# Kernel optimization log

Measured on AMD Instinct MI355X. Metric: run time of the kernel, lower is better.

The kernel has to match this reference:

```python
import jax, jax.numpy as jnp
import numpy as np

N, E, R, G = 50000, 800000, 8, 128
IN_EMBD, LAYER, OUT = 64, 256, 256
CARDS = [33, 5, 3, 4, 2, 3]
EPS = 1e-5


def setup_inputs() -> dict:
    key = jax.random.key(0)
    ks = iter(jax.random.split(key, 40))
    d = {}
    # int inputs
    cols = [jax.random.randint(next(ks), (N,), 0, c) for c in CARDS]
    d['x'] = jnp.stack(cols, axis=1)                                  # [N,6]
    d['edge_index'] = jax.random.randint(next(ks), (2, E), 0, N)      # [2,E]
    d['edge_type'] = jax.random.randint(next(ks), (E,), 0, R)         # [E]
    d['batch'] = jnp.sort(jax.random.randint(next(ks), (N,), 0, G))   # [N]
    # embedding tables
    for i, c in enumerate(CARDS):
        d[f'emb{i}'] = jax.random.normal(next(ks), (c, IN_EMBD), jnp.float32)
    # RGCNConv1
    d['W1'] = jax.random.normal(next(ks), (R, 6 * IN_EMBD, LAYER), jnp.float32) * 0.05
    d['root1'] = jax.random.normal(next(ks), (6 * IN_EMBD, LAYER), jnp.float32) * 0.05
    d['b1'] = jnp.zeros((LAYER,), jnp.float32)
    # RGCNConv2
    d['W2'] = jax.random.normal(next(ks), (R, LAYER, OUT), jnp.float32) * 0.05
    d['root2'] = jax.random.normal(next(ks), (LAYER, OUT), jnp.float32) * 0.05
    d['b2'] = jnp.zeros((OUT,), jnp.float32)
    # gate_nn: Linear -> BatchNorm1d -> ReLU -> Linear(.,1)
    d['Wg1'] = jax.random.normal(next(ks), (OUT, OUT), jnp.float32) * 0.05
    d['bg1'] = jnp.zeros((OUT,), jnp.float32)
    d['gamma'] = jnp.ones((OUT,), jnp.float32)
    d['beta'] = jnp.zeros((OUT,), jnp.float32)
    d['Wg2'] = jax.random.normal(next(ks), (OUT, 1), jnp.float32) * 0.05
    d['bg2'] = jnp.zeros((1,), jnp.float32)
    # graph head
    d['Wgl'] = jax.random.normal(next(ks), (OUT, 1), jnp.float32) * 0.05
    d['bgl'] = jnp.zeros((1,), jnp.float32)
    return d


def rgcn_conv(h, src, dst, etype, W, root, b):
    # per-relation transform of all nodes, then gather per edge (avoids per-edge weight gather)
    hr = jnp.einsum('ni,rio->rno', h, W)            # [R,N,out]
    msg = hr[etype, src]                             # [E,out]
    # mean aggregation per (dst, relation), matching PyG RGCNConv default aggr='mean'
    counts = jnp.zeros((h.shape[0], W.shape[0]), h.dtype).at[dst, etype].add(1.0)
    norm = 1.0 / jnp.clip(counts, 1.0)               # [N,R]
    agg = jax.ops.segment_sum(msg * norm[dst, etype][:, None], dst, num_segments=h.shape[0])
    return agg + h @ root + b


def global_attention(x, batch, Wg1, bg1, gamma, beta, Wg2, bg2):
    h = x @ Wg1 + bg1
    mu = jnp.mean(h, axis=0)
    var = jnp.var(h, axis=0)
    h = (h - mu) * jax.lax.rsqrt(var + EPS) * gamma + beta   # BatchNorm1d (batch stats)
    gate = jax.nn.relu(h) @ Wg2 + bg2                        # [N,1]
    gmax = jax.ops.segment_max(gate, batch, num_segments=G)
    e = jnp.exp(gate - gmax[batch])
    denom = jax.ops.segment_sum(e, batch, num_segments=G)
    alpha = e / denom[batch]
    return jax.ops.segment_sum(alpha * x, batch, num_segments=G)  # [G,out]


def reference(x, edge_index, edge_type, batch,
              emb0, emb1, emb2, emb3, emb4, emb5,
              W1, root1, b1, W2, root2, b2,
              Wg1, bg1, gamma, beta, Wg2, bg2, Wgl, bgl):
    tables = [emb0, emb1, emb2, emb3, emb4, emb5]
    h = jnp.concatenate([tables[i][x[:, i]] for i in range(6)], axis=1)  # [N, 6*in_embd]
    src, dst = edge_index[0], edge_index[1]
    h = jax.nn.sigmoid(rgcn_conv(h, src, dst, edge_type, W1, root1, b1))
    h = jax.nn.sigmoid(rgcn_conv(h, src, dst, edge_type, W2, root2, b2))
    pooled = global_attention(h, batch, Wg1, bg1, gamma, beta, Wg2, bg2)
    return jax.nn.sigmoid(pooled @ Wgl + bgl)  # [G,1]
```

## Files before the change

### kernel.cpp

```cpp
#include <hip/hip_runtime.h>
#include <hip/hip_bf16.h>
#include <cstdint>

#define NN 50000
#define EE 800000
#define RR 8
#define GG 128
#define D0 384
#define DL 256
#define NCR 50

typedef __attribute__((ext_vector_type(8))) short bf16x8;
typedef __attribute__((ext_vector_type(4))) float f32x4;

__device__ __forceinline__ float sigmoidf_(float x) { return 1.0f / (1.0f + expf(-x)); }

__device__ __forceinline__ ushort f2bf(float f) {
    uint u = __float_as_uint(f);
    u += 0x7fffu + ((u >> 16) & 1u);
    return (ushort)(u >> 16);
}
__device__ __forceinline__ uint pack2bf(float lo, float hi) {
    return (uint)f2bf(lo) | ((uint)f2bf(hi) << 16);
}
__device__ __forceinline__ float bf2f(ushort u) {
    return __uint_as_float((uint)u << 16);
}

__device__ __forceinline__ void accw8(float* s, uint4 a, float w) {
    s[0] += w * __uint_as_float(a.x << 16);
    s[1] += w * __uint_as_float(a.x & 0xffff0000u);
    s[2] += w * __uint_as_float(a.y << 16);
    s[3] += w * __uint_as_float(a.y & 0xffff0000u);
    s[4] += w * __uint_as_float(a.z << 16);
    s[5] += w * __uint_as_float(a.z & 0xffff0000u);
    s[6] += w * __uint_as_float(a.w << 16);
    s[7] += w * __uint_as_float(a.w & 0xffff0000u);
}

__device__ __forceinline__ void unp8(float* f, uint4 a) {
    f[0] = __uint_as_float(a.x << 16);
    f[1] = __uint_as_float(a.x & 0xffff0000u);
    f[2] = __uint_as_float(a.y << 16);
    f[3] = __uint_as_float(a.y & 0xffff0000u);
    f[4] = __uint_as_float(a.z << 16);
    f[5] = __uint_as_float(a.z & 0xffff0000u);
    f[6] = __uint_as_float(a.w << 16);
    f[7] = __uint_as_float(a.w & 0xffff0000u);
}
__device__ __forceinline__ uint4 pack8bf(const float* f) {
    uint4 p;
    p.x = pack2bf(f[0], f[1]);
    p.y = pack2bf(f[2], f[3]);
    p.z = pack2bf(f[4], f[5]);
    p.w = pack2bf(f[6], f[7]);
    return p;
}

__device__ __forceinline__ unsigned fenc(float x) {
    unsigned u = __float_as_uint(x);
    return (u & 0x80000000u) ? ~u : (u | 0x80000000u);
}
__device__ __forceinline__ float fdec(unsigned u) {
    unsigned b = (u & 0x80000000u) ? (u & 0x7fffffffu) : ~u;
    return __uint_as_float(b);
}

__global__ __launch_bounds__(256) void lutbuild_kernel(
    const float* __restrict__ e0, const float* __restrict__ e1,
    const float* __restrict__ e2, const float* __restrict__ e3,
    const float* __restrict__ e4, const float* __restrict__ e5,
    const float* __restrict__ W1, const float* __restrict__ root1,
    ushort* __restrict__ T)
{
    int b = blockIdx.x;
    int cr = b / 9;
    int r  = b - cr * 9;
    int t, c;
    if      (cr < 33) { t = 0; c = cr; }
    else if (cr < 38) { t = 1; c = cr - 33; }
    else if (cr < 41) { t = 2; c = cr - 38; }
    else if (cr < 45) { t = 3; c = cr - 41; }
    else if (cr < 47) { t = 4; c = cr - 45; }
    else              { t = 5; c = cr - 47; }
    const float* emb;
    switch (t) {
        case 0: emb = e0; break; case 1: emb = e1; break; case 2: emb = e2; break;
        case 3: emb = e3; break; case 4: emb = e4; break; default: emb = e5; break;
    }
    const float* er = emb + c * 64;
    int col = threadIdx.x;
    const float* Wb = (r < 8) ? (W1 + ((size_t)r * D0 + t * 64) * DL + col)
                              : (root1 + (size_t)(t * 64) * DL + col);
    float s = 0.f;
    #pragma unroll 8
    for (int k = 0; k < 64; k++) s += er[k] * Wb[(size_t)k * DL];
    T[(size_t)(cr * 9 + r) * DL + col] = f2bf(s);
}

__global__ __launch_bounds__(256) void gather_lut(
    const ushort* __restrict__ T,
    const int* __restrict__ x,
    const int2* __restrict__ epk,
    const int* __restrict__ offs,
    ushort* __restrict__ hacc,
    int r0, int first)
{
    constexpr int STR = 72;
    __shared__ ushort Ts[4 * NCR * STR];
    const int q = blockIdx.y;
    int t = threadIdx.x;
    for (int i = t; i < 4 * NCR * 8; i += 256) {
        int row = i >> 3, j = i & 7;
        int r = row / NCR, cr = row - r * NCR;
        uint4 v = *(const uint4*)&T[(size_t)(cr * 9 + r0 + r) * 256 + q * 64 + j * 8];
        *(uint4*)&Ts[row * STR + j * 8] = v;
    }
    __syncthreads();

    const int slot = t >> 3;
    const int l    = t & 7;
    const int c    = l * 8;

    int n = blockIdx.x * 32 + slot;
    if (n >= NN) return;
    int e    = offs[n * 8 + r0];
    int endE = (r0 + 4 == 8) ? ((n == NN - 1) ? EE : offs[n * 8 + 8])
                             : offs[n * 8 + r0 + 4];

    float acc[8];
    if (first) {
        #pragma unroll
        for (int qq = 0; qq < 8; qq++) acc[qq] = 0.f;
    } else {
        uint4 a = *(const uint4*)&hacc[(size_t)n * DL + q * 64 + c];
        unp8(acc, a);
    }

    const int cumc[6] = {0, 33, 38, 41, 45, 47};
    for (; e < endE; e += 2) {
        int e1 = min(e + 1, endE - 1);
        int2 p0 = epk[e], p1 = epk[e1];
        float w0 = __int_as_float(p0.y);
        float w1 = (e + 1 < endE) ? __int_as_float(p1.y) : 0.f;
        int s0 = p0.x >> 3, ra = (p0.x & 7) - r0;
        int s1 = p1.x >> 3, rb = (p1.x & 7) - r0;
        const int* xp0 = x + s0 * 6;
        const int* xp1 = x + s1 * 6;
        int cra[6], crb[6];
        #pragma unroll
        for (int tb = 0; tb < 6; tb++) { cra[tb] = cumc[tb] + xp0[tb]; }
        #pragma unroll
        for (int tb = 0; tb < 6; tb++) { crb[tb] = cumc[tb] + xp1[tb]; }
        #pragma unroll
        for (int tb = 0; tb < 6; tb++) {
            uint4 v = *(const uint4*)&Ts[(ra * NCR + cra[tb]) * STR + c];
            accw8(acc, v, w0);
        }
        #pragma unroll
        for (int tb = 0; tb < 6; tb++) {
            uint4 v = *(const uint4*)&Ts[(rb * NCR + crb[tb]) * STR + c];
            accw8(acc, v, w1);
        }
    }

    *(uint4*)&hacc[(size_t)n * DL + q * 64 + c] = pack8bf(acc);
}

__global__ __launch_bounds__(256) void lutfin_kernel(
    const ushort* __restrict__ T, const int* __restrict__ x,
    const ushort* __restrict__ hacc, const float* __restrict__ b1,
    ushort* __restrict__ h1)
{
    __shared__ ushort Ts[NCR * 256];
    int t = threadIdx.x;
    for (int i = t; i < NCR * 256; i += 256) {
        int cr = i >> 8, col = i & 255;
        Ts[i] = T[(size_t)(cr * 9 + 8) * 256 + col];
    }
    __syncthreads();

    const int slot = t >> 5;
    const int l = t & 31;
    const int c = l * 8;

    for (int base = blockIdx.x * 8; base < NN; base += gridDim.x * 8) {
        int n = base + slot;
        if (n < NN) {
            const int* xp = x + n * 6;
            const int cumc[6] = {0, 33, 38, 41, 45, 47};
            float acc[8];
            float4 b0 = *(const float4*)&b1[c];
            float4 bb = *(const float4*)&b1[c + 4];
            acc[0] = b0.x; acc[1] = b0.y; acc[2] = b0.z; acc[3] = b0.w;
            acc[4] = bb.x; acc[5] = bb.y; acc[6] = bb.z; acc[7] = bb.w;
            #pragma unroll
            for (int tb = 0; tb < 6; tb++) {
                int cr = cumc[tb] + xp[tb];
                uint4 v = *(const uint4*)&Ts[cr * 256 + c];
                accw8(acc, v, 1.0f);
            }
            uint4 hv = *(const uint4*)&hacc[(size_t)n * DL + c];
            float hf[8]; unp8(hf, hv);
            #pragma unroll
            for (int q = 0; q < 8; q++) acc[q] = sigmoidf_(acc[q] + hf[q]);
            *(uint4*)&h1[(size_t)n * DL + c] = pack8bf(acc);
        }
    }
}

__global__ __launch_bounds__(256) void cvtT_kernel(
    const float* __restrict__ W, const float* __restrict__ root,
    ushort* __restrict__ WbT, int nrel, int IN)
{
    int idx = blockIdx.x * 256 + threadIdx.x;
    int tot = (nrel + 1) * DL * IN;
    if (idx >= tot) return;
    int k = idx % IN;
    int rn = idx / IN;
    int n = rn % DL;
    int r = rn / DL;
    float v = (r < nrel) ? W[((size_t)r * IN + k) * DL + n] : root[(size_t)k * DL + n];
    WbT[idx] = f2bf(v);
}

__global__ __launch_bounds__(256) void count_kernel(
    const int* __restrict__ dst, const int* __restrict__ et, int* __restrict__ counts)
{
    int i = blockIdx.x * 256 + threadIdx.x;
    if (i < EE) atomicAdd(&counts[dst[i] * RR + et[i]], 1);
}

#define SCAN_CHUNK 4096
__global__ __launch_bounds__(256) void scanA_kernel(const int* __restrict__ cnt, int M, int* __restrict__ blkSums)
{
    __shared__ int s[256];
    int b = blockIdx.x, t = threadIdx.x;
    int base = b * SCAN_CHUNK + t * 16;
    int tot = 0;
    #pragma unroll
    for (int i = 0; i < 16; i++) { int idx = base + i; if (idx < M) tot += cnt[idx]; }
    s[t] = tot; __syncthreads();
    for (int off = 128; off > 0; off >>= 1) {
        if (t < off) s[t] += s[t + off];
        __syncthreads();
    }
    if (t == 0) blkSums[b] = s[0];
}

__global__ void scanB_kernel(const int* __restrict__ blkSums, int NB, int* __restrict__ blkOff)
{
    int l = threadIdx.x;
    int a = (l < NB) ? blkSums[l] : 0;
    int b = (64 + l < NB) ? blkSums[64 + l] : 0;
    int ia = a, ib = b;
    for (int o = 1; o < 64; o <<= 1) {
        int t0 = __shfl_up(ia, o, 64);
        if (l >= o) ia += t0;
        int t1 = __shfl_up(ib, o, 64);
        if (l >= o) ib += t1;
    }
    int tot0 = __shfl(ia, 63, 64);
    if (l < NB) blkOff[l] = ia - a;
    if (64 + l < NB) blkOff[64 + l] = tot0 + ib - b;
}

__global__ __launch_bounds__(256) void scanC_kernel(
    const int* __restrict__ cnt, int M, const int* __restrict__ blkOff,
    int* __restrict__ offs, int* __restrict__ curs)
{
    __shared__ int s[256];
    int b = blockIdx.x, t = threadIdx.x;
    int base = b * SCAN_CHUNK + t * 16;
    int loc[16];
    int tot = 0;
    #pragma unroll
    for (int i = 0; i < 16; i++) {
        int idx = base + i;
        int v = (idx < M) ? cnt[idx] : 0;
        loc[i] = tot; tot += v;
    }
    s[t] = tot; __syncthreads();
    for (int off = 1; off < 256; off <<= 1) {
        int v = (t >= off) ? s[t - off] : 0;
        __syncthreads();
        s[t] += v;
        __syncthreads();
    }
    int texc = s[t] - tot;
    int bb = blkOff[b];
    #pragma unroll
    for (int i = 0; i < 16; i++) {
        int idx = base + i;
        if (idx < M) { int o = bb + texc + loc[i]; offs[idx] = o; curs[idx] = o; }
    }
}

__global__ __launch_bounds__(256) void scatter_kernel(
    const int* __restrict__ src, const int* __restrict__ dst, const int* __restrict__ et,
    const int* __restrict__ cnts, int* __restrict__ cursors,
    int2* __restrict__ epk)
{
    int i = blockIdx.x * 256 + threadIdx.x;
    if (i < EE) {
        int r = et[i];
        int b = dst[i] * RR + r;
        int pos = atomicAdd(&cursors[b], 1);
        int2 p;
        p.x = src[i] * 8 + r;
        p.y = __float_as_int(1.0f / (float)cnts[b]);
        epk[pos] = p;
    }
}

template<int K, int MODE>
__global__ __launch_bounds__(256) void dense_gemm(
    const ushort* __restrict__ A,
    const ushort* __restrict__ Bt,
    const float* __restrict__ bias,
    const ushort* __restrict__ haccp,
    ushort* __restrict__ C,
    int M, int NCOL)
{
    constexpr int NKT = K / 64;
    __shared__ __attribute__((aligned(16))) ushort Al[2][128 * 64];
    __shared__ __attribute__((aligned(16))) ushort Bl[2][128 * 64];

    const int nwg  = gridDim.x * gridDim.y;
    const int flat = blockIdx.y * gridDim.x + blockIdx.x;
    const int q8 = nwg >> 3, r8 = nwg & 7;
    const int xcd = flat & 7, pos = flat >> 3;
    const int vid = ((xcd < r8) ? xcd * (q8 + 1) : r8 * (q8 + 1) + (xcd - r8) * q8) + pos;
    const int m0  = (vid / gridDim.x) * 128;
    const int n0  = (vid % gridDim.x) * 128;

    const int t    = threadIdx.x;
    const int lane = t & 63;
    const int wv   = t >> 6;
    const int wr   = (wv >> 1) * 64;
    const int wc   = (wv & 1) * 64;
    const int l15  = lane & 15;
    const int kg   = lane >> 4;

    const int sr = t >> 3;
    const int sc = (t & 7) * 8;
    const int g0 = sc,      g1 = sc + 4;
    const int s0 = ((g0 >> 5) << 2) + ((g0 & 15) >> 2), h0_ = (g0 >> 4) & 1;
    const int s1 = ((g1 >> 5) << 2) + ((g1 & 15) >> 2), h1_ = (g1 >> 4) & 1;

    int arow[4], brow[4];
    #pragma unroll
    for (int i = 0; i < 4; i++) {
        int r = sr + i * 32;
        arow[i] = min(m0 + r, M - 1);
        brow[i] = n0 + r;
    }

    uint4 av[4], bv[4];
    auto SLOAD = [&](int kt) {
        const ushort* Ak = A + kt * 64 + sc;
        const ushort* Bk = Bt + kt * 64 + sc;
        #pragma unroll
        for (int i = 0; i < 4; i++) av[i] = *(const uint4*)(Ak + (size_t)arow[i] * K);
        #pragma unroll
        for (int i = 0; i < 4; i++) bv[i] = *(const uint4*)(Bk + (size_t)brow[i] * K);
    };
    auto SWRITE = [&](int buf) {
        #pragma unroll
        for (int i = 0; i < 4; i++) {
            int row = sr + i * 32;
            int rx  = row & 7;
            int o0  = row * 64 + (((s0 ^ rx) << 3) + h0_ * 4);
            int o1  = row * 64 + (((s1 ^ rx) << 3) + h1_ * 4);
            *(uint2*)&Al[buf][o0] = make_uint2(av[i].x, av[i].y);
            *(uint2*)&Al[buf][o1] = make_uint2(av[i].z, av[i].w);
            *(uint2*)&Bl[buf][o0] = make_uint2(bv[i].x, bv[i].y);
            *(uint2*)&Bl[buf][o1] = make_uint2(bv[i].z, bv[i].w);
        }
    };

    f32x4 acc[4][4];
    #pragma unroll
    for (int mt = 0; mt < 4; mt++)
        #pragma unroll
        for (int nt = 0; nt < 4; nt++) acc[mt][nt] = (f32x4){0.f, 0.f, 0.f, 0.f};

    union FR { bf16x8 v; uint u[4]; };

    SLOAD(0);
    SWRITE(0);
    __syncthreads();

    for (int kt = 0; kt < NKT; kt++) {
        const int cur = kt & 1;
        if (kt + 1 < NKT) {
            SLOAD(kt + 1);
            __builtin_amdgcn_sched_barrier(0);
        }
        const ushort* Ap = Al[cur];
        const ushort* Bp = Bl[cur];
        #pragma unroll
        for (int kb = 0; kb < 2; kb++) {
            const int s = kb * 4 + kg;
            FR a[4], b[4];
            #pragma unroll
            for (int mt = 0; mt < 4; mt++) {
                int row = wr + mt * 16 + l15;
                uint4 va = *(const uint4*)&Ap[row * 64 + ((s ^ (row & 7)) << 3)];
                a[mt].u[0] = va.x; a[mt].u[1] = va.y; a[mt].u[2] = va.z; a[mt].u[3] = va.w;
            }
            #pragma unroll
            for (int nt = 0; nt < 4; nt++) {
                int row = wc + nt * 16 + l15;
                uint4 vb = *(const uint4*)&Bp[row * 64 + ((s ^ (row & 7)) << 3)];
                b[nt].u[0] = vb.x; b[nt].u[1] = vb.y; b[nt].u[2] = vb.z; b[nt].u[3] = vb.w;
            }
            #pragma unroll
            for (int nt = 0; nt < 4; nt++)
                #pragma unroll
                for (int mt = 0; mt < 4; mt++)
                    acc[mt][nt] = __builtin_amdgcn_mfma_f32_16x16x32_bf16(a[mt].v, b[nt].v, acc[mt][nt], 0, 0, 0);
        }
        if (kt + 1 < NKT) {
            SWRITE(cur ^ 1);
            __syncthreads();
        }
    }

    #pragma unroll
    for (int nt = 0; nt < 4; nt++) {
        int col = n0 + wc + nt * 16 + l15;
        float bvv = (MODE >= 1) ? bias[col] : 0.f;
        #pragma unroll
        for (int mt = 0; mt < 4; mt++) {
            #pragma unroll
            for (int i = 0; i < 4; i++) {
                int row = m0 + wr + mt * 16 + kg * 4 + i;
                if (row < M) {
                    float v = acc[mt][nt][i] + bvv;
                    if (MODE == 2) {
                        v += bf2f(haccp[(size_t)row * DL + col]);
                        v = sigmoidf_(v);
                    }
                    C[(size_t)row * NCOL + col] = f2bf(v);
                }
            }
        }
    }
}

__global__ __launch_bounds__(256) void gather_acc(
    const ushort* __restrict__ hrc,
    const int2* __restrict__ epk,
    const int* __restrict__ offs,
    ushort* __restrict__ hacc,
    int relStart, int relEnd, int first, int chc, int mask)
{
    int t = threadIdx.x;
    int slot = t >> 5;
    int l = t & 31;
    int n = blockIdx.x * 8 + slot;
    if (n >= NN) return;
    int e    = offs[n * 8 + relStart];
    int endE = (relEnd == 8 && n == NN - 1) ? EE : offs[n * 8 + relEnd];
    int c = l * 8;

    float acc[8];
    if (first) {
        #pragma unroll
        for (int q = 0; q < 8; q++) acc[q] = 0.f;
    } else {
        uint4 a = *(const uint4*)&hacc[(size_t)n * DL + c];
        unp8(acc, a);
    }

    for (; e < endE; e += 4) {
        int e1 = min(e + 1, endE - 1);
        int e2 = min(e + 2, endE - 1);
        int e3 = min(e + 3, endE - 1);
        int2 p0 = epk[e], p1 = epk[e1], p2 = epk[e2], p3 = epk[e3];
        float w0 = __int_as_float(p0.y);
        float w1 = (e + 1 < endE) ? __int_as_float(p1.y) : 0.f;
        float w2 = (e + 2 < endE) ? __int_as_float(p2.y) : 0.f;
        float w3 = (e + 3 < endE) ? __int_as_float(p3.y) : 0.f;
        int i0 = (p0.x >> 3) * chc + ((p0.x & 7) & mask) * DL;
        int i1 = (p1.x >> 3) * chc + ((p1.x & 7) & mask) * DL;
        int i2 = (p2.x >> 3) * chc + ((p2.x & 7) & mask) * DL;
        int i3 = (p3.x >> 3) * chc + ((p3.x & 7) & mask) * DL;
        uint4 v0 = *(const uint4*)&hrc[(size_t)i0 + c];
        uint4 v1 = *(const uint4*)&hrc[(size_t)i1 + c];
        uint4 v2 = *(const uint4*)&hrc[(size_t)i2 + c];
        uint4 v3 = *(const uint4*)&hrc[(size_t)i3 + c];
        accw8(acc, v0, w0); accw8(acc, v1, w1);
        accw8(acc, v2, w2); accw8(acc, v3, w3);
    }

    *(uint4*)&hacc[(size_t)n * DL + c] = pack8bf(acc);
}

__global__ __launch_bounds__(256) void bnstats_kernel(
    const ushort* __restrict__ hg1, float* __restrict__ colsum, float* __restrict__ colsum2)
{
    __shared__ float ss[8][256], ss2[8][256];
    int t = threadIdx.x;
    int g = t >> 5, l = t & 31;
    int c = l * 8;
    constexpr int RPB = (NN + 255) / 256;
    int row0 = blockIdx.x * RPB;
    int rend = min(row0 + RPB, NN);
    float s[8], s2[8];
    #pragma unroll
    for (int q = 0; q < 8; q++) { s[q] = 0.f; s2[q] = 0.f; }
    for (int r = row0 + g; r < rend; r += 8) {
        uint4 v = *(const uint4*)&hg1[(size_t)r * DL + c];
        float f[8]; unp8(f, v);
        #pragma unroll
        for (int q = 0; q < 8; q++) { s[q] += f[q]; s2[q] += f[q] * f[q]; }
    }
    #pragma unroll
    for (int q = 0; q < 8; q++) { ss[g][c + q] = s[q]; ss2[g][c + q] = s2[q]; }
    __syncthreads();
    float ts = 0.f, ts2 = 0.f;
    #pragma unroll
    for (int gg = 0; gg < 8; gg++) { ts += ss[gg][t]; ts2 += ss2[gg][t]; }
    atomicAdd(&colsum[t], ts);
    atomicAdd(&colsum2[t], ts2);
}

__global__ void bnfinal_kernel(
    const float* __restrict__ colsum, const float* __restrict__ colsum2,
    const float* __restrict__ gamma, float* __restrict__ mu, float* __restrict__ aa)
{
    int c = threadIdx.x;
    if (c < DL) {
        float m = colsum[c] / (float)NN;
        float var = colsum2[c] / (float)NN - m * m;
        mu[c] = m;
        aa[c] = rsqrtf(var + 1e-5f) * gamma[c];
    }
}

__global__ __launch_bounds__(256) void gate_kernel(
    const ushort* __restrict__ hg1, const float* __restrict__ mu,
    const float* __restrict__ aa, const float* __restrict__ beta,
    const float* __restrict__ Wg2, const float* __restrict__ bg2,
    const int* __restrict__ batch,
    float* __restrict__ gate, unsigned* __restrict__ gmaxu)
{
    int lane = threadIdx.x & 63;
    int wid = (blockIdx.x * blockDim.x + threadIdx.x) >> 6;
    int nw = (gridDim.x * blockDim.x) >> 6;
    int per = (NN + nw - 1) / nw;
    int n0 = wid * per;
    if (n0 >= NN) return;
    int n1 = min(n0 + per, NN);
    float bg2v = bg2[0];
    float lmax = -3.4e38f;
    int curb = batch[n0];
    for (int n = n0; n < n1; n++) {
        float s = 0.f;
        #pragma unroll
        for (int c = 0; c < 4; c++) {
            int d = c * 64 + lane;
            float v = bf2f(hg1[(size_t)n * DL + d]);
            float xn = (v - mu[d]) * aa[d] + beta[d];
            xn = fmaxf(xn, 0.f);
            s += xn * Wg2[d];
        }
        #pragma unroll
        for (int o = 32; o > 0; o >>= 1) s += __shfl_down(s, o, 64);
        if (lane == 0) {
            float g = s + bg2v;
            gate[n] = g;
            int b = batch[n];
            if (b != curb) {
                atomicMax(&gmaxu[curb], fenc(lmax));
                lmax = -3.4e38f; curb = b;
            }
            lmax = fmaxf(lmax, g);
        }
    }
    if (lane == 0) atomicMax(&gmaxu[curb], fenc(lmax));
}

__global__ __launch_bounds__(256) void expdenom_kernel(
    const float* __restrict__ gate, const int* __restrict__ batch,
    const unsigned* __restrict__ gmaxu, float* __restrict__ ealpha, float* __restrict__ denom)
{
    int tid = blockIdx.x * 256 + threadIdx.x;
    int i0 = tid * 4;
    if (i0 >= NN) return;
    int i1 = min(i0 + 4, NN);
    int curb = batch[i0];
    float m = fdec(gmaxu[curb]);
    float lsum = 0.f;
    for (int i = i0; i < i1; i++) {
        int b = batch[i];
        if (b != curb) {
            atomicAdd(&denom[curb], lsum);
            lsum = 0.f; curb = b; m = fdec(gmaxu[b]);
        }
        float ex = expf(gate[i] - m);
        ealpha[i] = ex;
        lsum += ex;
    }
    atomicAdd(&denom[curb], lsum);
}

__global__ __launch_bounds__(256) void pool_kernel(
    const ushort* __restrict__ h2, const float* __restrict__ ealpha,
    const float* __restrict__ denom, const int* __restrict__ batch,
    float* __restrict__ pooled)
{
    int t = threadIdx.x;
    int g = t >> 5, l = t & 31;
    int c = l * 8;
    int row0 = blockIdx.x * 128 + g * 16;
    if (row0 >= NN) return;
    int rend = min(row0 + 16, NN);
    float acc[8];
    #pragma unroll
    for (int q = 0; q < 8; q++) acc[q] = 0.f;
    int curg = batch[row0];
    for (int r = row0; r < rend; r++) {
        int gb = batch[r];
        if (gb != curg) {
            float inv = 1.0f / denom[curg];
            #pragma unroll
            for (int q = 0; q < 8; q++) atomicAdd(&pooled[curg * DL + c + q], acc[q] * inv);
            #pragma unroll
            for (int q = 0; q < 8; q++) acc[q] = 0.f;
            curg = gb;
        }
        float w = ealpha[r];
        uint4 v = *(const uint4*)&h2[(size_t)r * DL + c];
        accw8(acc, v, w);
    }
    float inv = 1.0f / denom[curg];
    #pragma unroll
    for (int q = 0; q < 8; q++) atomicAdd(&pooled[curg * DL + c + q], acc[q] * inv);
}

__global__ void head_kernel(
    const float* __restrict__ pooled, const float* __restrict__ Wgl,
    const float* __restrict__ bgl, float* __restrict__ out)
{
    int g = blockIdx.x;
    int lane = threadIdx.x;
    float s = 0.f;
    #pragma unroll
    for (int c = 0; c < 4; c++) {
        int d = c * 64 + lane;
        s += pooled[g * DL + d] * Wgl[d];
    }
    #pragma unroll
    for (int o = 32; o > 0; o >>= 1) s += __shfl_down(s, o, 64);
    if (lane == 0) out[g] = sigmoidf_(s + bgl[0]);
}

extern "C" void kernel_launch(void* const* d_in, const int* in_sizes, int n_in,
                              void* d_out, int out_size, void* d_ws, size_t ws_size,
                              hipStream_t stream)
{
    const int* x      = (const int*)d_in[0];
    const int* ei     = (const int*)d_in[1];
    const int* etype  = (const int*)d_in[2];
    const int* batch  = (const int*)d_in[3];
    const float* e0   = (const float*)d_in[4];
    const float* e1   = (const float*)d_in[5];
    const float* e2   = (const float*)d_in[6];
    const float* e3   = (const float*)d_in[7];
    const float* e4   = (const float*)d_in[8];
    const float* e5   = (const float*)d_in[9];
    const float* W1   = (const float*)d_in[10];
    const float* root1= (const float*)d_in[11];
    const float* b1   = (const float*)d_in[12];
    const float* W2   = (const float*)d_in[13];
    const float* root2= (const float*)d_in[14];
    const float* b2   = (const float*)d_in[15];
    const float* Wg1  = (const float*)d_in[16];
    const float* bg1  = (const float*)d_in[17];
    const float* gamma= (const float*)d_in[18];
    const float* beta = (const float*)d_in[19];
    const float* Wg2  = (const float*)d_in[20];
    const float* bg2  = (const float*)d_in[21];
    const float* Wgl  = (const float*)d_in[22];
    const float* bgl  = (const float*)d_in[23];
    float* out = (float*)d_out;

    const int* esrc_in = ei;
    const int* edst_in = ei + EE;

    char* ws = (char*)d_ws;
    size_t off = 0;
    auto alloc = [&](size_t b) -> char* {
        char* p = ws + off;
        off += (b + 255) & ~(size_t)255;
        return p;
    };
    ushort* h2     = (ushort*)alloc((size_t)NN * DL * 2);
    ushort* h1     = (ushort*)alloc((size_t)NN * DL * 2);
    ushort* hacc   = (ushort*)alloc((size_t)NN * DL * 2);
    size_t zstart = off;
    int*      counts  = (int*)alloc((size_t)NN * RR * 4);
    float*    colsum  = (float*)alloc(DL * 4);
    float*    colsum2 = (float*)alloc(DL * 4);
    unsigned* gmaxu   = (unsigned*)alloc(GG * 4);
    float*    denom   = (float*)alloc(GG * 4);
    float*    pooled  = (float*)alloc((size_t)GG * DL * 4);
    size_t zbytes = off - zstart;
    int*   offs    = (int*)alloc((size_t)NN * RR * 4);
    int*   cursors = (int*)alloc((size_t)NN * RR * 4);
    int2*  epk     = (int2*)alloc((size_t)EE * 8);
    int*   blkSums = (int*)alloc(512);
    int*   blkOff  = (int*)alloc(512);
    float* mu      = (float*)alloc(DL * 4);
    float* aa      = (float*)alloc(DL * 4);
    float* gate    = (float*)alloc((size_t)NN * 4);
    float* ealpha  = (float*)alloc((size_t)NN * 4);
    ushort* Tlut   = (ushort*)alloc((size_t)NCR * 9 * DL * 2);
    ushort* WbT2   = (ushort*)alloc((size_t)9 * DL * DL * 2);
    ushort* WbTg   = (ushort*)alloc((size_t)1 * DL * DL * 2);

    int npc;
    ushort* hrc;
    {
        size_t need4 = ((size_t)NN * 4 * DL * 2 + 255) & ~(size_t)255;
        size_t need2 = ((size_t)NN * 2 * DL * 2 + 255) & ~(size_t)255;
        if (off + need4 <= ws_size)      { npc = 4; hrc = (ushort*)alloc((size_t)NN * 4 * DL * 2); }
        else if (off + need2 <= ws_size) { npc = 2; hrc = (ushort*)alloc((size_t)NN * 2 * DL * 2); }
        else return;
    }
    const int chc = npc * DL;

    ushort* hg1 = hrc;

    hipMemsetAsync(ws + zstart, 0, zbytes, stream);

    lutbuild_kernel<<<NCR * 9, 256, 0, stream>>>(e0, e1, e2, e3, e4, e5, W1, root1, Tlut);
    count_kernel<<<(EE + 255) / 256, 256, 0, stream>>>(edst_in, etype, counts);
    {
        int tot2 = 9 * DL * DL;
        cvtT_kernel<<<(tot2 + 255) / 256, 256, 0, stream>>>(W2, root2, WbT2, RR, DL);
        int totg = 1 * DL * DL;
        cvtT_kernel<<<(totg + 255) / 256, 256, 0, stream>>>(nullptr, Wg1, WbTg, 0, DL);
    }

    const int M = NN * RR;
    const int NB = (M + SCAN_CHUNK - 1) / SCAN_CHUNK;
    scanA_kernel<<<NB, 256, 0, stream>>>(counts, M, blkSums);
    scanB_kernel<<<1, 64, 0, stream>>>(blkSums, NB, blkOff);
    scanC_kernel<<<NB, 256, 0, stream>>>(counts, M, blkOff, offs, cursors);
    scatter_kernel<<<(EE + 255) / 256, 256, 0, stream>>>(esrc_in, edst_in, etype, counts, cursors, epk);

    const int MT = (NN + 127) / 128;
    const dim3 GC(npc * 2, MT), G2(2, MT);
    const int ABLK = (NN + 7) / 8;

    {
        dim3 GL((NN + 31) / 32, 4);
        gather_lut<<<GL, 256, 0, stream>>>(Tlut, x, epk, offs, hacc, 0, 1);
        gather_lut<<<GL, 256, 0, stream>>>(Tlut, x, epk, offs, hacc, 4, 0);
    }
    lutfin_kernel<<<512, 256, 0, stream>>>(Tlut, x, hacc, b1, h1);

    for (int c0 = 0; c0 < RR; c0 += npc) {
        dense_gemm<DL, 0><<<GC, 256, 0, stream>>>(h1, WbT2 + (size_t)c0 * DL * DL, nullptr, nullptr, hrc, NN, chc);
        gather_acc<<<ABLK, 256, 0, stream>>>(hrc, epk, offs, hacc, c0, c0 + npc, c0 == 0, chc, npc - 1);
    }
    dense_gemm<DL, 2><<<G2, 256, 0, stream>>>(h1, WbT2 + (size_t)8 * DL * DL, b2, hacc, h2, NN, DL);

    dense_gemm<DL, 1><<<G2, 256, 0, stream>>>(h2, WbTg, bg1, nullptr, hg1, NN, DL);

    bnstats_kernel<<<256, 256, 0, stream>>>(hg1, colsum, colsum2);
    bnfinal_kernel<<<1, 256, 0, stream>>>(colsum, colsum2, gamma, mu, aa);
    gate_kernel<<<512, 256, 0, stream>>>(hg1, mu, aa, beta, Wg2, bg2, batch, gate, gmaxu);
    expdenom_kernel<<<((NN + 3) / 4 + 255) / 256, 256, 0, stream>>>(gate, batch, gmaxu, ealpha, denom);
    pool_kernel<<<(NN + 127) / 128, 256, 0, stream>>>(h2, ealpha, denom, batch, pooled);
    head_kernel<<<GG, 64, 0, stream>>>(pooled, Wgl, bgl, out);
}
```

Measured before the change: 638.5 us.

## Recast layer-1 RGCN as per-node category-count matrix times LUT GEMM in fp16

Layer 1 used to gather LUT rows per edge from shared memory. It now builds, for each node, a 9x50 matrix of weighted category counts over relations and the root (padded to K=512), and multiplies it by a transposed LUT with an fp16 MFMA GEMM that fuses bias and sigmoid. This replaces the per-edge 256-wide gather-accumulate with a scalar scatter of counts followed by a compact tensor-core GEMM. The LUT is stored in fp16 to keep precision for the counts, and the count build uses a large per-thread shared-memory row, which may limit occupancy.

```diff
diff --git a/kernel.cpp b/kernel.cpp
--- a/kernel.cpp
+++ b/kernel.cpp
@@ -9,8 +9,10 @@
 #define D0 384
 #define DL 256
 #define NCR 50
+#define KL1 512
 
 typedef __attribute__((ext_vector_type(8))) short bf16x8;
+typedef __attribute__((ext_vector_type(8))) _Float16 f16x8;
 typedef __attribute__((ext_vector_type(4))) float f32x4;
 
 __device__ __forceinline__ float sigmoidf_(float x) { return 1.0f / (1.0f + expf(-x)); }
@@ -25,6 +27,13 @@
 }
 __device__ __forceinline__ float bf2f(ushort u) {
     return __uint_as_float((uint)u << 16);
+}
+__device__ __forceinline__ ushort f2h(float f) {
+    _Float16 h = (_Float16)f;
+    return *(ushort*)&h;
+}
+__device__ __forceinline__ uint pack2h(float lo, float hi) {
+    return (uint)f2h(lo) | ((uint)f2h(hi) << 16);
 }
 
 __device__ __forceinline__ void accw8(float* s, uint4 a, float w) {
@@ -95,117 +104,66 @@
     float s = 0.f;
     #pragma unroll 8
     for (int k = 0; k < 64; k++) s += er[k] * Wb[(size_t)k * DL];
-    T[(size_t)(cr * 9 + r) * DL + col] = f2bf(s);
-}
-
-__global__ __launch_bounds__(256) void gather_lut(
-    const ushort* __restrict__ T,
+    T[(size_t)(cr * 9 + r) * DL + col] = f2h(s);
+}
+
+__global__ __launch_bounds__(256) void btl1_kernel(
+    const ushort* __restrict__ T, ushort* __restrict__ Bt)
+{
+    int idx = blockIdx.x * 256 + threadIdx.x;
+    if (idx >= 256 * KL1) return;
+    int col = idx / KL1, k = idx - col * KL1;
+    ushort v = 0;
+    if (k < 450) {
+        int rr = k / 50, cr = k - rr * 50;
+        v = T[(size_t)(cr * 9 + rr) * 256 + col];
+    }
+    Bt[idx] = v;
+}
+
+__global__ __launch_bounds__(256) void cntbuild_kernel(
     const int* __restrict__ x,
     const int2* __restrict__ epk,
     const int* __restrict__ offs,
-    ushort* __restrict__ hacc,
-    int r0, int first)
-{
-    constexpr int STR = 72;
-    __shared__ ushort Ts[4 * NCR * STR];
-    const int q = blockIdx.y;
-    int t = threadIdx.x;
-    for (int i = t; i < 4 * NCR * 8; i += 256) {
-        int row = i >> 3, j = i & 7;
-        int r = row / NCR, cr = row - r * NCR;
-        uint4 v = *(const uint4*)&T[(size_t)(cr * 9 + r0 + r) * 256 + q * 64 + j * 8];
-        *(uint4*)&Ts[row * STR + j * 8] = v;
-    }
-    __syncthreads();
-
-    const int slot = t >> 3;
-    const int l    = t & 7;
-    const int c    = l * 8;
-
-    int n = blockIdx.x * 32 + slot;
+    ushort* __restrict__ A)
+{
+    __shared__ float Ls[256 * 53];
+    int t  = threadIdx.x;
+    int id = blockIdx.x * 256 + t;
+    int n  = id / 9;
+    int rr = id - n * 9;
     if (n >= NN) return;
-    int e    = offs[n * 8 + r0];
-    int endE = (r0 + 4 == 8) ? ((n == NN - 1) ? EE : offs[n * 8 + 8])
-                             : offs[n * 8 + r0 + 4];
-
-    float acc[8];
-    if (first) {
-        #pragma unroll
-        for (int qq = 0; qq < 8; qq++) acc[qq] = 0.f;
+    float* row = &Ls[t * 53];
+    #pragma unroll
+    for (int j = 0; j < 50; j++) row[j] = 0.f;
+    const int cumc[6] = {0, 33, 38, 41, 45, 47};
+
+    if (rr < 8) {
+        int b  = n * 8 + rr;
+        int e0 = offs[b];
+        int e1 = (b + 1 < NN * 8) ? offs[b + 1] : EE;
+        for (int e = e0; e < e1; e++) {
+            int2 p = epk[e];
+            int s = p.x >> 3;
+            float w = __int_as_float(p.y);
+            const int* xp = x + s * 6;
+            #pragma unroll
+            for (int tb = 0; tb < 6; tb++) row[cumc[tb] + xp[tb]] += w;
+        }
     } else {
-        uint4 a = *(const uint4*)&hacc[(size_t)n * DL + q * 64 + c];
-        unp8(acc, a);
-    }
-
-    const int cumc[6] = {0, 33, 38, 41, 45, 47};
-    for (; e < endE; e += 2) {
-        int e1 = min(e + 1, endE - 1);
-        int2 p0 = epk[e], p1 = epk[e1];
-        float w0 = __int_as_float(p0.y);
-        float w1 = (e + 1 < endE) ? __int_as_float(p1.y) : 0.f;
-        int s0 = p0.x >> 3, ra = (p0.x & 7) - r0;
-        int s1 = p1.x >> 3, rb = (p1.x & 7) - r0;
-        const int* xp0 = x + s0 * 6;
-        const int* xp1 = x + s1 * 6;
-        int cra[6], crb[6];
-        #pragma unroll
-        for (int tb = 0; tb < 6; tb++) { cra[tb] = cumc[tb] + xp0[tb]; }
-        #pragma unroll
-        for (int tb = 0; tb < 6; tb++) { crb[tb] = cumc[tb] + xp1[tb]; }
-        #pragma unroll
-        for (int tb = 0; tb < 6; tb++) {
-            uint4 v = *(const uint4*)&Ts[(ra * NCR + cra[tb]) * STR + c];
-            accw8(acc, v, w0);
-        }
-        #pragma unroll
-        for (int tb = 0; tb < 6; tb++) {
-            uint4 v = *(const uint4*)&Ts[(rb * NCR + crb[tb]) * STR + c];
-            accw8(acc, v, w1);
-        }
-    }
-
-    *(uint4*)&hacc[(size_t)n * DL + q * 64 + c] = pack8bf(acc);
-}
-
-__global__ __launch_bounds__(256) void lutfin_kernel(
-    const ushort* __restrict__ T, const int* __restrict__ x,
-    const ushort* __restrict__ hacc, const float* __restrict__ b1,
-    ushort* __restrict__ h1)
-{
-    __shared__ ushort Ts[NCR * 256];
-    int t = threadIdx.x;
-    for (int i = t; i < NCR * 256; i += 256) {
-        int cr = i >> 8, col = i & 255;
-        Ts[i] = T[(size_t)(cr * 9 + 8) * 256 + col];
-    }
-    __syncthreads();
-
-    const int slot = t >> 5;
-    const int l = t & 31;
-    const int c = l * 8;
-
-    for (int base = blockIdx.x * 8; base < NN; base += gridDim.x * 8) {
-        int n = base + slot;
-        if (n < NN) {
-            const int* xp = x + n * 6;
-            const int cumc[6] = {0, 33, 38, 41, 45, 47};
-            float acc[8];
-            float4 b0 = *(const float4*)&b1[c];
-            float4 bb = *(const float4*)&b1[c + 4];
-            acc[0] = b0.x; acc[1] = b0.y; acc[2] = b0.z; acc[3] = b0.w;
-            acc[4] = bb.x; acc[5] = bb.y; acc[6] = bb.z; acc[7] = bb.w;
-            #pragma unroll
-            for (int tb = 0; tb < 6; tb++) {
-                int cr = cumc[tb] + xp[tb];
-                uint4 v = *(const uint4*)&Ts[cr * 256 + c];
-                accw8(acc, v, 1.0f);
-            }
-            uint4 hv = *(const uint4*)&hacc[(size_t)n * DL + c];
-            float hf[8]; unp8(hf, hv);
-            #pragma unroll
-            for (int q = 0; q < 8; q++) acc[q] = sigmoidf_(acc[q] + hf[q]);
-            *(uint4*)&h1[(size_t)n * DL + c] = pack8bf(acc);
-        }
+        const int* xp = x + n * 6;
+        #pragma unroll
+        for (int tb = 0; tb < 6; tb++) row[cumc[tb] + xp[tb]] += 1.f;
+    }
+
+    ushort* dst = A + (size_t)n * KL1 + rr * 50;
+    #pragma unroll
+    for (int j = 0; j < 50; j += 2)
+        *(uint*)&dst[j] = pack2h(row[j], row[j + 1]);
+    if (rr == 8) {
+        ushort* pz = A + (size_t)n * KL1 + 450;
+        #pragma unroll
+        for (int j = 0; j < 62; j += 2) *(uint*)&pz[j] = 0u;
     }
 }
 
@@ -313,7 +271,7 @@
     }
 }
 
-template<int K, int MODE>
+template<int K, int MODE, int DT>
 __global__ __launch_bounds__(256) void dense_gemm(
     const ushort* __restrict__ A,
     const ushort* __restrict__ Bt,
@@ -385,7 +343,7 @@
         #pragma unroll
         for (int nt = 0; nt < 4; nt++) acc[mt][nt] = (f32x4){0.f, 0.f, 0.f, 0.f};
 
-    union FR { bf16x8 v; uint u[4]; };
+    union FR { bf16x8 v; f16x8 h; uint u[4]; };
 
     SLOAD(0);
     SWRITE(0);
@@ -418,8 +376,12 @@
             #pragma unroll
             for (int nt = 0; nt < 4; nt++)
                 #pragma unroll
-                for (int mt = 0; mt < 4; mt++)
-                    acc[mt][nt] = __builtin_amdgcn_mfma_f32_16x16x32_bf16(a[mt].v, b[nt].v, acc[mt][nt], 0, 0, 0);
+                for (int mt = 0; mt < 4; mt++) {
+                    if (DT == 0)
+                        acc[mt][nt] = __builtin_amdgcn_mfma_f32_16x16x32_bf16(a[mt].v, b[nt].v, acc[mt][nt], 0, 0, 0);
+                    else
+                        acc[mt][nt] = __builtin_amdgcn_mfma_f32_16x16x32_f16(a[mt].h, b[nt].h, acc[mt][nt], 0, 0, 0);
+                }
         }
         if (kt + 1 < NKT) {
             SWRITE(cur ^ 1);
@@ -442,6 +404,7 @@
                         v += bf2f(haccp[(size_t)row * DL + col]);
                         v = sigmoidf_(v);
                     }
+                    if (MODE == 3) v = sigmoidf_(v);
                     C[(size_t)row * NCOL + col] = f2bf(v);
                 }
             }
@@ -719,6 +682,7 @@
     float* gate    = (float*)alloc((size_t)NN * 4);
     float* ealpha  = (float*)alloc((size_t)NN * 4);
     ushort* Tlut   = (ushort*)alloc((size_t)NCR * 9 * DL * 2);
+    ushort* BtL1   = (ushort*)alloc((size_t)DL * KL1 * 2);
     ushort* WbT2   = (ushort*)alloc((size_t)9 * DL * DL * 2);
     ushort* WbTg   = (ushort*)alloc((size_t)1 * DL * DL * 2);
 
@@ -732,12 +696,13 @@
         else return;
     }
     const int chc = npc * DL;
-
-    ushort* hg1 = hrc;
+    ushort* cnt50 = hrc;
+    ushort* hg1   = hrc;
 
     hipMemsetAsync(ws + zstart, 0, zbytes, stream);
 
     lutbuild_kernel<<<NCR * 9, 256, 0, stream>>>(e0, e1, e2, e3, e4, e5, W1, root1, Tlut);
+    btl1_kernel<<<(256 * KL1 + 255) / 256, 256, 0, stream>>>(Tlut, BtL1);
     count_kernel<<<(EE + 255) / 256, 256, 0, stream>>>(edst_in, etype, counts);
     {
         int tot2 = 9 * DL * DL;
@@ -757,20 +722,16 @@
     const dim3 GC(npc * 2, MT), G2(2, MT);
     const int ABLK = (NN + 7) / 8;
 
-    {
-        dim3 GL((NN + 31) / 32, 4);
-        gather_lut<<<GL, 256, 0, stream>>>(Tlut, x, epk, offs, hacc, 0, 1);
-        gather_lut<<<GL, 256, 0, stream>>>(Tlut, x, epk, offs, hacc, 4, 0);
-    }
-    lutfin_kernel<<<512, 256, 0, stream>>>(Tlut, x, hacc, b1, h1);
+    cntbuild_kernel<<<(NN * 9 + 255) / 256, 256, 0, stream>>>(x, epk, offs, cnt50);
+    dense_gemm<KL1, 3, 1><<<G2, 256, 0, stream>>>(cnt50, BtL1, b1, nullptr, h1, NN, DL);
 
     for (int c0 = 0; c0 < RR; c0 += npc) {
-        dense_gemm<DL, 0><<<GC, 256, 0, stream>>>(h1, WbT2 + (size_t)c0 * DL * DL, nullptr, nullptr, hrc, NN, chc);
+        dense_gemm<DL, 0, 0><<<GC, 256, 0, stream>>>(h1, WbT2 + (size_t)c0 * DL * DL, nullptr, nullptr, hrc, NN, chc);
         gather_acc<<<ABLK, 256, 0, stream>>>(hrc, epk, offs, hacc, c0, c0 + npc, c0 == 0, chc, npc - 1);
     }
-    dense_gemm<DL, 2><<<G2, 256, 0, stream>>>(h1, WbT2 + (size_t)8 * DL * DL, b2, hacc, h2, NN, DL);
-
-    dense_gemm<DL, 1><<<G2, 256, 0, stream>>>(h2, WbTg, bg1, nullptr, hg1, NN, DL);
+    dense_gemm<DL, 2, 0><<<G2, 256, 0, stream>>>(h1, WbT2 + (size_t)8 * DL * DL, b2, hacc, h2, NN, DL);
+
+    dense_gemm<DL, 1, 0><<<G2, 256, 0, stream>>>(h2, WbTg, bg1, nullptr, hg1, NN, DL);
 
     bnstats_kernel<<<256, 256, 0, stream>>>(hg1, colsum, colsum2);
     bnfinal_kernel<<<1, 256, 0, stream>>>(colsum, colsum2, gamma, mu, aa);
```

Measured after the change: 554.5 us. -13.2%, faster.
